# Kernel tuning notes

Measured on AMD Instinct MI355X. Metric: run time of the kernel, lower is better.

Reference implementation:

```python
import jax, jax.numpy as jnp
import numpy as np

D_MODEL = 1024
NUM_HEADS = 16
D_FF = 4096
SEQ = 2048
BATCH = 2
THETA = 10000.0
EPS = 1e-5


def _param(key, shape, fan_in, fan_out):
    std = 2.0 / (fan_in + fan_out) ** 0.5
    return std * jax.random.truncated_normal(key, -3.0, 3.0, shape, dtype=jnp.float32)


def setup_inputs() -> dict:
    key = jax.random.key(0)
    ks = jax.random.split(key, 8)
    d, h, f = D_MODEL, NUM_HEADS, D_FF
    return {
        'x': jax.random.normal(ks[0], (BATCH, SEQ, d), dtype=jnp.float32),
        'token_positions': jnp.arange(SEQ, dtype=jnp.int32),
        'wq': _param(ks[1], (d, d), d, d),
        'wk': _param(ks[2], (d, d), d, d),
        'wv': _param(ks[3], (d, d), d, d),
        'wo': _param(ks[4], (d, d), d, d),
        'ln1_w': jnp.ones((d,), jnp.float32),
        'ln2_w': jnp.ones((d,), jnp.float32),
        'w1': _param(ks[5], (f, d), d, f),
        'w2': _param(ks[6], (d, f), f, d),
        'w3': _param(ks[7], (f, d), d, f),
    }


def rmsnorm(x, w):
    x32 = x.astype(jnp.float32)
    rms = jnp.sqrt(jnp.mean(x32 * x32, axis=-1, keepdims=True) + EPS)
    return ((x32 / rms) * w).astype(x.dtype)


def apply_rope(x, cos, sin):
    # x: [b, h, s, d_k]; cos/sin: [s, d_k//2] -> broadcast as [1,1,s,d_k//2]
    xe, xo = x[..., ::2], x[..., 1::2]
    c = cos[None, None, :, :]
    s = sin[None, None, :, :]
    re = xe * c - xo * s
    ro = xe * s + xo * c
    return jnp.stack((re, ro), axis=-1).reshape(x.shape)


def block_forward(x, token_positions, wq, wk, wv, wo, ln1_w, ln2_w, w1, w2, w3):
    b, s, d = x.shape
    h = NUM_HEADS
    dk = d // h
    # RoPE tables at token positions
    inv_freq = 1.0 / (THETA ** (jnp.arange(0, dk // 2, dtype=jnp.float32) * 2.0 / dk))
    freqs = token_positions.astype(jnp.float32)[:, None] * inv_freq[None, :]  # [s, dk/2]
    cos, sin = jnp.cos(freqs), jnp.sin(freqs)

    # --- attention sublayer (pre-norm) ---
    xn = rmsnorm(x, ln1_w)
    q = jnp.einsum('bsd,ed->bse', xn, wq).reshape(b, s, h, dk).transpose(0, 2, 1, 3)
    k = jnp.einsum('bsd,ed->bse', xn, wk).reshape(b, s, h, dk).transpose(0, 2, 1, 3)
    v = jnp.einsum('bsd,ed->bse', xn, wv).reshape(b, s, h, dk).transpose(0, 2, 1, 3)
    q = apply_rope(q, cos, sin)
    k = apply_rope(k, cos, sin)
    scores = jnp.einsum('bhqd,bhkd->bhqk', q, k) / jnp.sqrt(jnp.float32(dk))
    causal = jnp.tril(jnp.ones((s, s), dtype=bool))
    scores = jnp.where(causal[None, None], scores, -jnp.inf)
    attn = jax.nn.softmax(scores, axis=-1)
    o = jnp.einsum('bhqk,bhkd->bhqd', attn, v)
    o = o.transpose(0, 2, 1, 3).reshape(b, s, d)
    x = x + jnp.einsum('bse,de->bsd', o, wo)

    # --- SwiGLU sublayer (pre-norm) ---
    xn = rmsnorm(x, ln2_w)
    x1 = jnp.einsum('bsd,fd->bsf', xn, w1)
    x3 = jnp.einsum('bsd,fd->bsf', xn, w3)
    gated = (x1 * jax.nn.sigmoid(x1)) * x3
    return x + jnp.einsum('bsf,df->bsd', gated, w2)


def reference(x, token_positions, wq, wk, wv, wo, ln1_w, ln2_w, w1, w2, w3):
    return block_forward(x, token_positions, wq, wk, wv, wo, ln1_w, ln2_w, w1, w2, w3)
```

## Files before the change

### kernel.cpp

```cpp
#include <hip/hip_runtime.h>
#include <hip/hip_bf16.h>

typedef __attribute__((ext_vector_type(4))) float f32x4;
typedef __attribute__((ext_vector_type(8))) short bf16x8;
typedef unsigned short u16;
typedef unsigned int u32;
typedef __attribute__((ext_vector_type(4))) u16 u16x4;

#define DEV static __device__ __forceinline__

constexpr int Bb = 2, Ss = 2048, Dd = 1024, Hh = 16, DKk = 64;
constexpr int Mm = Bb * Ss;

DEV float bf2f(u16 u) { union { u32 i; float f; } v; v.i = (u32)u << 16; return v.f; }
DEV u16 f2bf(float f) {
  union { float f; u32 i; } v; v.f = f;
  u32 r = v.i + 0x7FFFu + ((v.i >> 16) & 1u);
  return (u16)(r >> 16);
}

DEV void gload_lds16(const u16* g, u16* l) {
  __builtin_amdgcn_global_load_lds((const __attribute__((address_space(1))) u32*)g,
                                   (__attribute__((address_space(3))) u32*)l, 16, 0, 0);
}

DEV int swz16(int o) {
  return o ^ (((o >> 8) & 1) << 6) ^ (((o >> 9) & 1) << 5);
}

__global__ __launch_bounds__(256) void k_prep(const float* __restrict__ wq, const float* __restrict__ wk,
                          const float* __restrict__ wv, const float* __restrict__ wo,
                          const float* __restrict__ w1, const float* __restrict__ w2,
                          const float* __restrict__ w3,
                          u16* __restrict__ wqkv, u16* __restrict__ wob,
                          u16* __restrict__ w13, u16* __restrict__ w2b,
                          const float* __restrict__ x, const float* __restrict__ ln1,
                          u16* __restrict__ xn) {
  if (blockIdx.x < 16384) {
    int i = (blockIdx.x * 256 + threadIdx.x) * 4;
    int seg = i >> 20;
    const float* src; u16* dst;
    if (seg == 0)      { src = wq + i;             dst = wqkv + i; }
    else if (seg == 1) { src = wk + (i - (1<<20)); dst = wqkv + i; }
    else if (seg == 2) { src = wv + (i - (2<<20)); dst = wqkv + i; }
    else if (seg == 3) { src = wo + (i - (3<<20)); dst = wob  + (i - (3<<20)); }
    else if (seg < 8)  {
      int ii = i - (4<<20);
      int ri = ii >> 10, ci = ii & 1023;
      int dr = ((ri >> 4) << 5) + (ri & 15);
      src = w1 + ii; dst = w13 + (long)dr * 1024 + ci;
    }
    else if (seg < 12) { src = w2 + (i - (8<<20)); dst = w2b  + (i - (8<<20)); }
    else {
      int ii = i - (12<<20);
      int ri = ii >> 10, ci = ii & 1023;
      int dr = ((ri >> 4) << 5) + 16 + (ri & 15);
      src = w3 + ii; dst = w13 + (long)dr * 1024 + ci;
    }
    float4 v = *(const float4*)src;
    u16x4 o = { f2bf(v.x), f2bf(v.y), f2bf(v.z), f2bf(v.w) };
    *(u16x4*)dst = o;
  } else {
    int row = blockIdx.x - 16384;
    int t = threadIdx.x;
    float4 v = ((const float4*)(x + (long)row * Dd))[t];
    float ss = v.x * v.x + v.y * v.y + v.z * v.z + v.w * v.w;
#pragma unroll
    for (int m = 32; m; m >>= 1) ss += __shfl_xor(ss, m, 64);
    __shared__ float red[4];
    if ((t & 63) == 0) red[t >> 6] = ss;
    __syncthreads();
    float tot = red[0] + red[1] + red[2] + red[3];
    float r = rsqrtf(tot * (1.0f / Dd) + 1e-5f);
    float4 wv2 = ((const float4*)ln1)[t];
    u16x4 o = { f2bf(v.x * r * wv2.x), f2bf(v.y * r * wv2.y),
                f2bf(v.z * r * wv2.z), f2bf(v.w * r * wv2.w) };
    ((u16x4*)(xn + (long)row * Dd))[t] = o;
  }
}

__global__ __launch_bounds__(256) void k_rmsnorm(const float* __restrict__ x,
                                                 const float* __restrict__ w,
                                                 u16* __restrict__ out) {
  int row = blockIdx.x;
  int t = threadIdx.x;
  float4 v = ((const float4*)(x + (long)row * Dd))[t];
  float ss = v.x * v.x + v.y * v.y + v.z * v.z + v.w * v.w;
#pragma unroll
  for (int m = 32; m; m >>= 1) ss += __shfl_xor(ss, m, 64);
  __shared__ float red[4];
  if ((t & 63) == 0) red[t >> 6] = ss;
  __syncthreads();
  float tot = red[0] + red[1] + red[2] + red[3];
  float r = rsqrtf(tot * (1.0f / Dd) + 1e-5f);
  float4 wv = ((const float4*)w)[t];
  u16x4 o = { f2bf(v.x * r * wv.x), f2bf(v.y * r * wv.y),
              f2bf(v.z * r * wv.z), f2bf(v.w * r * wv.w) };
  ((u16x4*)(out + (long)row * Dd))[t] = o;
}

__global__ void k_rope(u16* __restrict__ q, u16* __restrict__ k, const int* __restrict__ tp) {
  int idx = blockIdx.x * 256 + threadIdx.x;
  if (idx >= Bb * Ss * Hh * 32) return;
  int p = idx & 31;
  int h = (idx >> 5) & 15;
  int row = idx >> 9;
  int s = row & (Ss - 1);
  float pos = (float)tp[s];
  float invf = __expf(-(float)p * (2.0f / DKk) * 9.2103403719761836f);
  float fr = pos * invf;
  float sn, cs;
  sincosf(fr, &sn, &cs);
  long base = (long)row * Dd + h * DKk + 2 * p;
  float xe = bf2f(q[base]), xo = bf2f(q[base + 1]);
  q[base]     = f2bf((xe * cs - xo * sn) * 0.125f);
  q[base + 1] = f2bf((xe * sn + xo * cs) * 0.125f);
  xe = bf2f(k[base]); xo = bf2f(k[base + 1]);
  k[base]     = f2bf(xe * cs - xo * sn);
  k[base + 1] = f2bf(xe * sn + xo * cs);
}

__global__ void k_addout4(const u16* __restrict__ p, const float* __restrict__ x2,
                          float* __restrict__ out) {
  int i = (blockIdx.x * 256 + threadIdx.x) * 4;
  float4 c = *(const float4*)(x2 + i);
  float s0 = c.x, s1 = c.y, s2 = c.z, s3 = c.w;
#pragma unroll
  for (int z = 0; z < 4; z++) {
    u16x4 a = *(const u16x4*)(p + (long)z * Mm * 1024 + i);
    s0 += bf2f(a[0]); s1 += bf2f(a[1]); s2 += bf2f(a[2]); s3 += bf2f(a[3]);
  }
  float4 o = { s0, s1, s2, s3 };
  *(float4*)(out + i) = o;
}

template <int OM, bool RES>
__global__ __launch_bounds__(256) void k_gemm(const u16* __restrict__ A,
                                              const u16* __restrict__ Bm,
                                              void* __restrict__ Cout,
                                              const float* __restrict__ Rres,
                                              int N, int Kl, int Kstr) {
  __shared__ u16 Abuf[128 * 32];
  __shared__ u16 Bbuf[128 * 32];
  const int tid = threadIdx.x;
  const int wid = tid >> 6, lane = tid & 63;
  const int wm = wid >> 1, wn = wid & 1;
  const int lq = lane >> 4, ll = lane & 15;
  const int lin = blockIdx.y * gridDim.x + blockIdx.x;
  const int c = lin & 7, j = lin >> 3;
  const int ncc = gridDim.x >> 2;
  const int bxc = (c % ncc) * 4 + (j & 3);
  const int byc = (c / ncc) * 8 + (j >> 2);
  const int m0 = byc * 128, n0 = bxc * 128;

  const u16* Ap = A + (long)blockIdx.z * Kl;
  const u16* Bp = Bm + (long)blockIdx.z * Kl;

  f32x4 acc[4][4] = {};

  const int srow = tid >> 2;
  const int scol = (tid & 3) * 8;
  const long aoff = (long)(m0 + srow) * Kstr + scol;
  const long boff = (long)(n0 + srow) * Kstr + scol;
  u16* aldsw = Abuf + wid * 512;
  u16* bldsw = Bbuf + wid * 512;

  for (int k0 = 0; k0 < Kl; k0 += 32) {
    __syncthreads();
    gload_lds16(Ap + aoff + k0, aldsw);
    gload_lds16(Ap + aoff + (long)64 * Kstr + k0, aldsw + 2048);
    gload_lds16(Bp + boff + k0, bldsw);
    gload_lds16(Bp + boff + (long)64 * Kstr + k0, bldsw + 2048);
    __syncthreads();
    bf16x8 af[4], bfr[4];
#pragma unroll
    for (int i = 0; i < 4; i++)
      af[i] = *(const bf16x8*)&Abuf[(wm * 64 + i * 16 + ll) * 32 + lq * 8];
#pragma unroll
    for (int j2 = 0; j2 < 4; j2++)
      bfr[j2] = *(const bf16x8*)&Bbuf[(wn * 64 + j2 * 16 + ll) * 32 + lq * 8];
#pragma unroll
    for (int i = 0; i < 4; i++)
#pragma unroll
      for (int j2 = 0; j2 < 4; j2++)
        acc[i][j2] = __builtin_amdgcn_mfma_f32_16x16x32_bf16(af[i], bfr[j2], acc[i][j2], 0, 0, 0);
  }

  float* fout = (float*)Cout + (long)blockIdx.z * Mm * (long)N;
#pragma unroll
  for (int i = 0; i < 4; i++) {
    const int rowb = m0 + wm * 64 + i * 16 + lq * 4;
#pragma unroll
    for (int j2 = 0; j2 < 4; j2++) {
      const int col = n0 + wn * 64 + j2 * 16 + ll;
#pragma unroll
      for (int r = 0; r < 4; r++) {
        int rr = rowb + r;
        float v = acc[i][j2][r];
        if (RES) v += Rres[(long)rr * N + col];
        if (OM == 1) {
          fout[(long)rr * N + col] = v;
        } else {
          ((u16*)Cout)[(long)rr * N + col] = f2bf(v);
        }
      }
    }
  }
}

#define STG_A(d, h, kt)                                                         \
  { gload_lds16(A + aoff[0] + (long)(h) * 128 * Kstr + (kt) * 64, &sA[d][h][dst0]); \
    gload_lds16(A + aoff[1] + (long)(h) * 128 * Kstr + (kt) * 64, &sA[d][h][dst1]); }
#define STG_B(d, h, kt)                                                         \
  { gload_lds16(Bm + boff[0] + (long)(h) * 128 * Kstr + (kt) * 64, &sB[d][h][dst0]); \
    gload_lds16(Bm + boff[1] + (long)(h) * 128 * Kstr + (kt) * 64, &sB[d][h][dst1]); }

#define PHASE(q, d, DOB, WVN, ...)                                              \
  {                                                                             \
    bf16x8 af_[2][2];                                                           \
    _Pragma("unroll") for (int s_ = 0; s_ < 2; s_++)                            \
    _Pragma("unroll") for (int kk_ = 0; kk_ < 2; kk_++) {                       \
      int ms_ = (q) * 4 + wm * 2 + s_;                                          \
      int lo_ = ((ms_ & 7) * 16 + ll) * 128 + kk_ * 64 + lq * 16;               \
      af_[s_][kk_] = *(const bf16x8*)((const char*)sA[d][ms_ >> 3] + swz16(lo_)); \
    }                                                                           \
    if (DOB) {                                                                  \
      _Pragma("unroll") for (int ns_ = 0; ns_ < 4; ns_++)                       \
      _Pragma("unroll") for (int kk_ = 0; kk_ < 2; kk_++) {                     \
        int rl_ = wn * 64 + ns_ * 16 + ll;                                      \
        int lo_ = (rl_ & 127) * 128 + kk_ * 64 + lq * 16;                       \
        bfr[ns_][kk_] = *(const bf16x8*)((const char*)sB[d][rl_ >> 7] + swz16(lo_)); \
      }                                                                         \
    }                                                                           \
    __VA_ARGS__;                                                                \
    __builtin_amdgcn_s_barrier();                                               \
    asm volatile("s_waitcnt lgkmcnt(0)" ::: "memory");                          \
    __builtin_amdgcn_sched_barrier(0);                                          \
    __builtin_amdgcn_s_setprio(1);                                              \
    _Pragma("unroll") for (int s_ = 0; s_ < 2; s_++)                            \
    _Pragma("unroll") for (int ns_ = 0; ns_ < 4; ns_++)                         \
    _Pragma("unroll") for (int kk_ = 0; kk_ < 2; kk_++)                         \
      acc[q][s_][ns_] = __builtin_amdgcn_mfma_f32_16x16x32_bf16(                \
          af_[s_][kk_], bfr[ns_][kk_], acc[q][s_][ns_], 0, 0, 0);               \
    __builtin_amdgcn_s_setprio(0);                                              \
    { int wv_ = (WVN);                                                          \
      if (wv_ == 6) { asm volatile("s_waitcnt vmcnt(6)" ::: "memory"); }        \
      else if (wv_ == 0) { asm volatile("s_waitcnt vmcnt(0)" ::: "memory"); } } \
    __builtin_amdgcn_s_barrier();                                               \
  }

template <int OM, int CW, int CH>
__global__ __launch_bounds__(512) void k_gemm8(const u16* __restrict__ A,
                                               const u16* __restrict__ Bm,
                                               void* __restrict__ Cout,
                                               int N, int Kl, int Kstr) {
  __shared__ u16 sA[2][2][8192];
  __shared__ u16 sB[2][2][8192];
  constexpr int NBPC = CW * CH;
  const int gx = gridDim.x;
  const int lin = blockIdx.y * gx + blockIdx.x;
  const int c = lin & 7;
  const int idx = lin >> 3;
  const int chunkid = c + 8 * (idx / NBPC);
  const int jj = idx % NBPC;
  const int ncc = gx / CW;
  const int bx = (chunkid % ncc) * CW + jj % CW;
  const int by = (chunkid / ncc) * CH + jj / CW;
  const long m0 = (long)by * 256, n0 = (long)bx * 256;
  const int tid = threadIdx.x;
  const int wid = tid >> 6, lane = tid & 63;
  const int wm = wid >> 2, wn = wid & 3;
  const int lq = lane >> 4, ll = lane & 15;
  const long zoff = (long)blockIdx.z * Kl;

  long aoff[2], boff[2];
#pragma unroll
  for (int j2 = 0; j2 < 2; j2++) {
    int off = j2 * 8192 + wid * 1024 + lane * 16;
    int lo = swz16(off);
    int r = lo >> 7, cc = (lo & 127) >> 1;
    aoff[j2] = (m0 + r) * Kstr + cc + zoff;
    boff[j2] = (n0 + r) * Kstr + cc + zoff;
  }
  const int dst0 = wid * 512;
  const int dst1 = 4096 + wid * 512;

  f32x4 acc[4][2][4] = {};
  bf16x8 bfr[4][2];

  const int NT = Kl >> 6;
  const int NI = NT >> 1;

  STG_A(0, 0, 0); STG_A(0, 1, 0); STG_B(0, 0, 0); STG_B(0, 1, 0);
  STG_B(1, 0, 1); STG_B(1, 1, 1); STG_A(1, 0, 1);
  asm volatile("s_waitcnt vmcnt(6)" ::: "memory");
  __builtin_amdgcn_s_barrier();

  for (int it = 0; it < NI; it++) {
    const int t = 2 * it;
    const bool full = (t + 2 < NT);
    PHASE(0, 0, true,  -1,            STG_A(1, 1, t + 1))
    PHASE(1, 0, false, -1,            if (full) STG_B(0, 0, t + 2))
    PHASE(2, 0, false, -1,            if (full) STG_B(0, 1, t + 2))
    PHASE(3, 0, false, full ? 6 : 0,  if (full) STG_A(0, 0, t + 2))
    PHASE(0, 1, true,  -1,            if (full) STG_A(0, 1, t + 2))
    PHASE(1, 1, false, -1,            if (full) STG_B(1, 0, t + 3))
    PHASE(2, 1, false, -1,            if (full) STG_B(1, 1, t + 3))
    PHASE(3, 1, false, full ? 6 : -1, if (full) STG_A(1, 0, t + 3))
  }

#pragma unroll
  for (int q = 0; q < 4; q++)
#pragma unroll
    for (int s = 0; s < 2; s++) {
      const long row0 = m0 + (q * 4 + wm * 2 + s) * 16 + lq * 4;
      if (OM == 7) {
#pragma unroll
        for (int n2 = 0; n2 < 2; n2++) {
          const long ocol = ((n0 + wn * 64) >> 1) + n2 * 16 + ll;
#pragma unroll
          for (int r = 0; r < 4; r++) {
            float v1 = acc[q][s][n2 * 2][r];
            float v3 = acc[q][s][n2 * 2 + 1][r];
            float g = v1 / (1.0f + __expf(-v1)) * v3;
            ((u16*)Cout)[(row0 + r) * 4096 + ocol] = f2bf(g);
          }
        }
      } else {
#pragma unroll
        for (int ns = 0; ns < 4; ns++) {
          const long col = n0 + wn * 64 + ns * 16 + ll;
#pragma unroll
          for (int r = 0; r < 4; r++) {
            float v = acc[q][s][ns][r];
            long rr = row0 + r;
            if (OM == 3) {
              if (col < 2048) {
                ((u16*)Cout)[(col >> 10) * (long)(Mm * 1024) + rr * 1024 + (col & 1023)] = f2bf(v);
              } else {
                int d = col & 63, hh = ((int)col >> 6) & 15;
                int b2 = (int)rr >> 11, s2 = (int)rr & (Ss - 1);
                ((u16*)Cout)[(long)(2 * Mm * 1024) + ((long)((b2 * Hh + hh) * DKk + d)) * Ss + s2] = f2bf(v);
              }
            } else {
              ((u16*)Cout)[(long)blockIdx.z * Mm * (long)N + rr * N + col] = f2bf(v);
            }
          }
        }
      }
    }
}

constexpr int PPAD = 80;

DEV void attn_tile(const u16* __restrict__ Kc, const u16* __restrict__ Vc,
                   u16* __restrict__ myP, const bf16x8* qf, f32x4* accO,
                   float* mrow, float* lrow, int qloc, bool diag, int lq, int ll) {
  f32x4 sacc[4] = {};
  __builtin_amdgcn_s_setprio(1);
#pragma unroll
  for (int fn = 0; fn < 4; fn++)
#pragma unroll
    for (int ks = 0; ks < 2; ks++) {
      bf16x8 kf = *(const bf16x8*)&Kc[(fn * 16 + ll) * 64 + (((ks * 4 + lq) ^ (ll & 7)) * 8)];
      sacc[fn] = __builtin_amdgcn_mfma_f32_16x16x32_bf16(qf[ks], kf, sacc[fn], 0, 0, 0);
    }
  __builtin_amdgcn_s_setprio(0);
  float sv[4][4], pmax[4];
#pragma unroll
  for (int r = 0; r < 4; r++) pmax[r] = -1e30f;
#pragma unroll
  for (int fn = 0; fn < 4; fn++) {
    int kc = fn * 16 + ll;
#pragma unroll
    for (int r = 0; r < 4; r++) {
      float v = sacc[fn][r];
      if (diag && kc > qloc + r) v = -1e30f;
      sv[fn][r] = v;
      pmax[r] = fmaxf(pmax[r], v);
    }
  }
#pragma unroll
  for (int r = 0; r < 4; r++) {
#pragma unroll
    for (int m = 1; m < 16; m <<= 1) pmax[r] = fmaxf(pmax[r], __shfl_xor(pmax[r], m, 64));
  }
  float alpha[4], rsum[4];
#pragma unroll
  for (int r = 0; r < 4; r++) {
    float mnew = fmaxf(mrow[r], pmax[r]);
    alpha[r] = __expf(mrow[r] - mnew);
    mrow[r] = mnew;
    rsum[r] = 0.f;
  }
#pragma unroll
  for (int fn = 0; fn < 4; fn++) {
#pragma unroll
    for (int r = 0; r < 4; r++) {
      float p = __expf(sv[fn][r] - mrow[r]);
      rsum[r] += p;
      myP[(lq * 4 + r) * PPAD + fn * 16 + ll] = f2bf(p);
    }
  }
#pragma unroll
  for (int r = 0; r < 4; r++) {
#pragma unroll
    for (int m = 1; m < 16; m <<= 1) rsum[r] += __shfl_xor(rsum[r], m, 64);
    lrow[r] = lrow[r] * alpha[r] + rsum[r];
  }
#pragma unroll
  for (int fn = 0; fn < 4; fn++)
#pragma unroll
    for (int r = 0; r < 4; r++) accO[fn][r] *= alpha[r];
  bf16x8 pa[2];
#pragma unroll
  for (int ks = 0; ks < 2; ks++)
    pa[ks] = *(const bf16x8*)&myP[ll * PPAD + ks * 32 + lq * 8];
  __builtin_amdgcn_s_setprio(1);
#pragma unroll
  for (int fn = 0; fn < 4; fn++)
#pragma unroll
    for (int ks = 0; ks < 2; ks++) {
      bf16x8 vf = *(const bf16x8*)&Vc[(fn * 16 + ll) * 64 + (((ks * 4 + lq) ^ (ll & 7)) * 8)];
      accO[fn] = __builtin_amdgcn_mfma_f32_16x16x32_bf16(pa[ks], vf, accO[fn], 0, 0, 0);
    }
  __builtin_amdgcn_s_setprio(0);
}

__global__ __launch_bounds__(256) void k_attn(const u16* __restrict__ Q,
                                              const u16* __restrict__ Kb,
                                              const u16* __restrict__ VT,
                                              u16* __restrict__ O) {
  __shared__ u16 Kt[2][64 * 64];
  __shared__ u16 Vt[2][64 * 64];
  __shared__ u16 P[4][16 * PPAD];
  const int pair = blockIdx.x;
  const int bh = blockIdx.y;
  const int b = bh >> 4, h = bh & 15;
  const int tid = threadIdx.x;
  const int wid = tid >> 6, lane = tid & 63;
  const int lq = lane >> 4, ll = lane & 15;
  const int qtA = pair, qtB = 31 - pair;
  const int qr0A = qtA * 64 + wid * 16;
  const int qr0B = qtB * 64 + wid * 16;
  const int qloc = wid * 16 + lq * 4;
  const long qkbase = ((long)b * Ss) * Dd + h * DKk;
  const long vbase  = ((long)(b * Hh + h) * DKk) * Ss;
  const int nk = 32 - pair;

  const int slot0 = wid * 64 + lane;
  const int r0 = slot0 >> 3, c0 = (slot0 & 7) ^ (r0 & 7);
  const int slot1 = 256 + slot0;
  const int r1 = slot1 >> 3, c1 = (slot1 & 7) ^ (r1 & 7);
  const int ldsb0 = (wid * 64) * 8;
  const int ldsb1 = (256 + wid * 64) * 8;

  bf16x8 qfA[2], qfB[2];
#pragma unroll
  for (int ks = 0; ks < 2; ks++) {
    qfA[ks] = *(const bf16x8*)&Q[qkbase + (long)(qr0A + ll) * Dd + ks * 32 + lq * 8];
    qfB[ks] = *(const bf16x8*)&Q[qkbase + (long)(qr0B + ll) * Dd + ks * 32 + lq * 8];
  }

  f32x4 accA[4] = {}, accB[4] = {};
  float mA[4], lA[4], mB[4], lB[4];
#pragma unroll
  for (int r = 0; r < 4; r++) { mA[r] = mB[r] = -1e30f; lA[r] = lB[r] = 0.f; }
  u16* myP = P[wid];

  gload_lds16(Kb + qkbase + (long)r0 * Dd + c0 * 8, Kt[0] + ldsb0);
  gload_lds16(Kb + qkbase + (long)r1 * Dd + c1 * 8, Kt[0] + ldsb1);
  gload_lds16(VT + vbase + (long)r0 * Ss + c0 * 8, Vt[0] + ldsb0);
  gload_lds16(VT + vbase + (long)r1 * Ss + c1 * 8, Vt[0] + ldsb1);
  __syncthreads();

  for (int kt = 0; kt < nk; kt++) {
    if (kt + 1 < nk) {
      const int kn = (kt + 1) * 64;
      u16* kd = Kt[(kt + 1) & 1];
      u16* vd = Vt[(kt + 1) & 1];
      gload_lds16(Kb + qkbase + (long)(kn + r0) * Dd + c0 * 8, kd + ldsb0);
      gload_lds16(Kb + qkbase + (long)(kn + r1) * Dd + c1 * 8, kd + ldsb1);
      gload_lds16(VT + vbase + (long)r0 * Ss + kn + c0 * 8, vd + ldsb0);
      gload_lds16(VT + vbase + (long)r1 * Ss + kn + c1 * 8, vd + ldsb1);
    }
    const u16* Kc = Kt[kt & 1];
    const u16* Vc = Vt[kt & 1];

    attn_tile(Kc, Vc, myP, qfB, accB, mB, lB, qloc, kt == nk - 1, lq, ll);
    if (kt <= pair)
      attn_tile(Kc, Vc, myP, qfA, accA, mA, lA, qloc, kt == pair, lq, ll);
    __syncthreads();
  }

#pragma unroll
  for (int fn = 0; fn < 4; fn++) {
#pragma unroll
    for (int r = 0; r < 4; r++) {
      int rowA = qr0A + lq * 4 + r;
      int rowB = qr0B + lq * 4 + r;
      O[((long)(b * Ss + rowA)) * Dd + h * DKk + fn * 16 + ll] = f2bf(accA[fn][r] / lA[r]);
      O[((long)(b * Ss + rowB)) * Dd + h * DKk + fn * 16 + ll] = f2bf(accB[fn][r] / lB[r]);
    }
  }
}

extern "C" void kernel_launch(void* const* d_in, const int* in_sizes, int n_in,
                              void* d_out, int out_size, void* d_ws, size_t ws_size,
                              hipStream_t stream) {
  const float* x   = (const float*)d_in[0];
  const int*   tp  = (const int*)d_in[1];
  const float* wq  = (const float*)d_in[2];
  const float* wk  = (const float*)d_in[3];
  const float* wv  = (const float*)d_in[4];
  const float* wo  = (const float*)d_in[5];
  const float* ln1 = (const float*)d_in[6];
  const float* ln2 = (const float*)d_in[7];
  const float* w1  = (const float*)d_in[8];
  const float* w2  = (const float*)d_in[9];
  const float* w3  = (const float*)d_in[10];

  char* ws = (char*)d_ws;
  const size_t MB = 1024 * 1024;
  u16*   wqkv_b = (u16*)(ws + 0 * MB);
  u16*   wo_b   = (u16*)(ws + 6 * MB);
  u16*   w13_b  = (u16*)(ws + 8 * MB);
  u16*   w2_b   = (u16*)(ws + 24 * MB);
  u16*   xn     = (u16*)(ws + 32 * MB);
  float* x2     = (float*)(ws + 40 * MB);
  u16*   qb     = (u16*)(ws + 56 * MB);
  u16*   kb     = (u16*)(ws + 64 * MB);
  u16*   vtb    = (u16*)(ws + 72 * MB);
  u16*   ob     = (u16*)(ws + 80 * MB);
  u16*   x1     = (u16*)(ws + 56 * MB);
  u16*   pparts = (u16*)(ws + 88 * MB);

  k_prep<<<16384 + Mm, 256, 0, stream>>>(wq, wk, wv, wo, w1, w2, w3,
                                         wqkv_b, wo_b, w13_b, w2_b, x, ln1, xn);
  k_gemm8<3, 3, 4><<<dim3(12, 16), 512, 0, stream>>>(xn, wqkv_b, qb, 3072, 1024, 1024);
  k_rope<<<(Bb * Ss * Hh * 32) / 256, 256, 0, stream>>>(qb, kb, tp);
  k_attn<<<dim3(16, 32), 256, 0, stream>>>(qb, kb, vtb, ob);
  k_gemm<1, true><<<dim3(8, 32), 256, 0, stream>>>(ob, wo_b, x2, x, 1024, 1024, 1024);
  k_rmsnorm<<<Mm, 256, 0, stream>>>(x2, ln2, xn);
  k_gemm8<7, 4, 4><<<dim3(32, 16), 512, 0, stream>>>(xn, w13_b, x1, 8192, 1024, 1024);
  k_gemm8<6, 4, 2><<<dim3(4, 16, 4), 512, 0, stream>>>(x1, w2_b, pparts, 1024, 1024, 4096);
  k_addout4<<<4096, 256, 0, stream>>>(pparts, x2, (float*)d_out);
}
```

Measured before the change: 319.6 us.

## Fuse RoPE into QKV GEMM epilogue and widen attention K/V tiles to 128

Removes the standalone RoPE kernel. k_prep now precomputes cos/sin tables, and the QKV GEMM epilogue applies the rotation (and the 0.125 Q scale) before storing, using a lane shuffle to fetch the paired element. This drops a full read-modify-write pass over Q and K plus a kernel launch. Separately, the attention kernel now stages 128-key K/V tiles per double-buffer stage, so there are half as many barriers and load phases, at the cost of doubled LDS usage. The shuffle-based pairing assumes adjacent columns sit in adjacent lanes in the MFMA output layout. The tables live in the x2 region, which is overwritten later.

```diff
diff --git a/kernel.cpp b/kernel.cpp
--- a/kernel.cpp
+++ b/kernel.cpp
@@ -35,7 +35,8 @@
                           u16* __restrict__ wqkv, u16* __restrict__ wob,
                           u16* __restrict__ w13, u16* __restrict__ w2b,
                           const float* __restrict__ x, const float* __restrict__ ln1,
-                          u16* __restrict__ xn) {
+                          u16* __restrict__ xn, const int* __restrict__ tp,
+                          float* __restrict__ ctab, float* __restrict__ stab) {
   if (blockIdx.x < 16384) {
     int i = (blockIdx.x * 256 + threadIdx.x) * 4;
     int seg = i >> 20;
@@ -60,7 +61,7 @@
     float4 v = *(const float4*)src;
     u16x4 o = { f2bf(v.x), f2bf(v.y), f2bf(v.z), f2bf(v.w) };
     *(u16x4*)dst = o;
-  } else {
+  } else if (blockIdx.x < 16384 + Mm) {
     int row = blockIdx.x - 16384;
     int t = threadIdx.x;
     float4 v = ((const float4*)(x + (long)row * Dd))[t];
@@ -76,6 +77,16 @@
     u16x4 o = { f2bf(v.x * r * wv2.x), f2bf(v.y * r * wv2.y),
                 f2bf(v.z * r * wv2.z), f2bf(v.w * r * wv2.w) };
     ((u16x4*)(xn + (long)row * Dd))[t] = o;
+  } else {
+    int e = (blockIdx.x - 16384 - Mm) * 256 + threadIdx.x;
+    int srow = e >> 5, p = e & 31;
+    float pos = (float)tp[srow];
+    float invf = __expf(-(float)p * (2.0f / DKk) * 9.2103403719761836f);
+    float fr = pos * invf;
+    float sn, cs;
+    sincosf(fr, &sn, &cs);
+    ctab[e] = cs;
+    stab[e] = sn;
   }
 }
 
@@ -97,27 +108,6 @@
   u16x4 o = { f2bf(v.x * r * wv.x), f2bf(v.y * r * wv.y),
               f2bf(v.z * r * wv.z), f2bf(v.w * r * wv.w) };
   ((u16x4*)(out + (long)row * Dd))[t] = o;
-}
-
-__global__ void k_rope(u16* __restrict__ q, u16* __restrict__ k, const int* __restrict__ tp) {
-  int idx = blockIdx.x * 256 + threadIdx.x;
-  if (idx >= Bb * Ss * Hh * 32) return;
-  int p = idx & 31;
-  int h = (idx >> 5) & 15;
-  int row = idx >> 9;
-  int s = row & (Ss - 1);
-  float pos = (float)tp[s];
-  float invf = __expf(-(float)p * (2.0f / DKk) * 9.2103403719761836f);
-  float fr = pos * invf;
-  float sn, cs;
-  sincosf(fr, &sn, &cs);
-  long base = (long)row * Dd + h * DKk + 2 * p;
-  float xe = bf2f(q[base]), xo = bf2f(q[base + 1]);
-  q[base]     = f2bf((xe * cs - xo * sn) * 0.125f);
-  q[base + 1] = f2bf((xe * sn + xo * cs) * 0.125f);
-  xe = bf2f(k[base]); xo = bf2f(k[base + 1]);
-  k[base]     = f2bf(xe * cs - xo * sn);
-  k[base + 1] = f2bf(xe * sn + xo * cs);
 }
 
 __global__ void k_addout4(const u16* __restrict__ p, const float* __restrict__ x2,
@@ -253,6 +243,8 @@
 __global__ __launch_bounds__(512) void k_gemm8(const u16* __restrict__ A,
                                                const u16* __restrict__ Bm,
                                                void* __restrict__ Cout,
+                                               const float* __restrict__ ctab,
+                                               const float* __restrict__ stab,
                                                int N, int Kl, int Kstr) {
   __shared__ u16 sA[2][2][8192];
   __shared__ u16 sB[2][2][8192];
@@ -335,12 +327,22 @@
             float v = acc[q][s][ns][r];
             long rr = row0 + r;
             if (OM == 3) {
+              float v2 = v;
               if (col < 2048) {
-                ((u16*)Cout)[(col >> 10) * (long)(Mm * 1024) + rr * 1024 + (col & 1023)] = f2bf(v);
+                int d = (int)col & 63;
+                int srow = (int)rr & (Ss - 1);
+                int p = d >> 1;
+                float cs = ctab[srow * 32 + p], sn = stab[srow * 32 + p];
+                float o = __shfl_xor(v, 1);
+                v2 = (d & 1) ? (o * sn + v * cs) : (v * cs - o * sn);
+                if (col < 1024) v2 *= 0.125f;
+              }
+              if (col < 2048) {
+                ((u16*)Cout)[(col >> 10) * (long)(Mm * 1024) + rr * 1024 + (col & 1023)] = f2bf(v2);
               } else {
                 int d = col & 63, hh = ((int)col >> 6) & 15;
                 int b2 = (int)rr >> 11, s2 = (int)rr & (Ss - 1);
-                ((u16*)Cout)[(long)(2 * Mm * 1024) + ((long)((b2 * Hh + hh) * DKk + d)) * Ss + s2] = f2bf(v);
+                ((u16*)Cout)[(long)(2 * Mm * 1024) + ((long)((b2 * Hh + hh) * DKk + d)) * Ss + s2] = f2bf(v2);
               }
             } else {
               ((u16*)Cout)[(long)blockIdx.z * Mm * (long)N + rr * N + col] = f2bf(v);
@@ -353,7 +355,7 @@
 
 constexpr int PPAD = 80;
 
-DEV void attn_tile(const u16* __restrict__ Kc, const u16* __restrict__ Vc,
+DEV void attn_tile(const u16* __restrict__ Kh, const u16* __restrict__ Vc, int vcb,
                    u16* __restrict__ myP, const bf16x8* qf, f32x4* accO,
                    float* mrow, float* lrow, int qloc, bool diag, int lq, int ll) {
   f32x4 sacc[4] = {};
@@ -362,7 +364,7 @@
   for (int fn = 0; fn < 4; fn++)
 #pragma unroll
     for (int ks = 0; ks < 2; ks++) {
-      bf16x8 kf = *(const bf16x8*)&Kc[(fn * 16 + ll) * 64 + (((ks * 4 + lq) ^ (ll & 7)) * 8)];
+      bf16x8 kf = *(const bf16x8*)&Kh[(fn * 16 + ll) * 64 + (((ks * 4 + lq) ^ (ll & 7)) * 8)];
       sacc[fn] = __builtin_amdgcn_mfma_f32_16x16x32_bf16(qf[ks], kf, sacc[fn], 0, 0, 0);
     }
   __builtin_amdgcn_s_setprio(0);
@@ -421,7 +423,7 @@
   for (int fn = 0; fn < 4; fn++)
 #pragma unroll
     for (int ks = 0; ks < 2; ks++) {
-      bf16x8 vf = *(const bf16x8*)&Vc[(fn * 16 + ll) * 64 + (((ks * 4 + lq) ^ (ll & 7)) * 8)];
+      bf16x8 vf = *(const bf16x8*)&Vc[(fn * 16 + ll) * 128 + (((vcb + ks * 4 + lq) ^ (ll & 7)) * 8)];
       accO[fn] = __builtin_amdgcn_mfma_f32_16x16x32_bf16(pa[ks], vf, accO[fn], 0, 0, 0);
     }
   __builtin_amdgcn_s_setprio(0);
@@ -431,8 +433,8 @@
                                               const u16* __restrict__ Kb,
                                               const u16* __restrict__ VT,
                                               u16* __restrict__ O) {
-  __shared__ u16 Kt[2][64 * 64];
-  __shared__ u16 Vt[2][64 * 64];
+  __shared__ u16 Kt[2][128 * 64];
+  __shared__ u16 Vt[2][64 * 128];
   __shared__ u16 P[4][16 * PPAD];
   const int pair = blockIdx.x;
   const int bh = blockIdx.y;
@@ -446,14 +448,17 @@
   const int qloc = wid * 16 + lq * 4;
   const long qkbase = ((long)b * Ss) * Dd + h * DKk;
   const long vbase  = ((long)(b * Hh + h) * DKk) * Ss;
-  const int nk = 32 - pair;
-
-  const int slot0 = wid * 64 + lane;
-  const int r0 = slot0 >> 3, c0 = (slot0 & 7) ^ (r0 & 7);
-  const int slot1 = 256 + slot0;
-  const int r1 = slot1 >> 3, c1 = (slot1 & 7) ^ (r1 & 7);
-  const int ldsb0 = (wid * 64) * 8;
-  const int ldsb1 = (256 + wid * 64) * 8;
+  const int nk64 = 32 - pair;
+  const int nk128 = (nk64 + 1) >> 1;
+
+  int kr[4], kc[4], vr[4], vc[4], ldsb[4];
+#pragma unroll
+  for (int i = 0; i < 4; i++) {
+    int s = 256 * i + wid * 64 + lane;
+    kr[i] = s >> 3;  kc[i] = (s & 7) ^ (kr[i] & 7);
+    vr[i] = s >> 4;  vc[i] = (s & 15) ^ (vr[i] & 7);
+    ldsb[i] = (256 * i + wid * 64) * 8;
+  }
 
   bf16x8 qfA[2], qfB[2];
 #pragma unroll
@@ -468,28 +473,36 @@
   for (int r = 0; r < 4; r++) { mA[r] = mB[r] = -1e30f; lA[r] = lB[r] = 0.f; }
   u16* myP = P[wid];
 
-  gload_lds16(Kb + qkbase + (long)r0 * Dd + c0 * 8, Kt[0] + ldsb0);
-  gload_lds16(Kb + qkbase + (long)r1 * Dd + c1 * 8, Kt[0] + ldsb1);
-  gload_lds16(VT + vbase + (long)r0 * Ss + c0 * 8, Vt[0] + ldsb0);
-  gload_lds16(VT + vbase + (long)r1 * Ss + c1 * 8, Vt[0] + ldsb1);
+#pragma unroll
+  for (int i = 0; i < 4; i++) {
+    gload_lds16(Kb + qkbase + (long)kr[i] * Dd + kc[i] * 8, Kt[0] + ldsb[i]);
+    gload_lds16(VT + vbase + (long)vr[i] * Ss + vc[i] * 8, Vt[0] + ldsb[i]);
+  }
   __syncthreads();
 
-  for (int kt = 0; kt < nk; kt++) {
-    if (kt + 1 < nk) {
-      const int kn = (kt + 1) * 64;
-      u16* kd = Kt[(kt + 1) & 1];
-      u16* vd = Vt[(kt + 1) & 1];
-      gload_lds16(Kb + qkbase + (long)(kn + r0) * Dd + c0 * 8, kd + ldsb0);
-      gload_lds16(Kb + qkbase + (long)(kn + r1) * Dd + c1 * 8, kd + ldsb1);
-      gload_lds16(VT + vbase + (long)r0 * Ss + kn + c0 * 8, vd + ldsb0);
-      gload_lds16(VT + vbase + (long)r1 * Ss + kn + c1 * 8, vd + ldsb1);
-    }
-    const u16* Kc = Kt[kt & 1];
-    const u16* Vc = Vt[kt & 1];
-
-    attn_tile(Kc, Vc, myP, qfB, accB, mB, lB, qloc, kt == nk - 1, lq, ll);
-    if (kt <= pair)
-      attn_tile(Kc, Vc, myP, qfA, accA, mA, lA, qloc, kt == pair, lq, ll);
+  for (int j = 0; j < nk128; j++) {
+    if (j + 1 < nk128) {
+      const int kn = (j + 1) * 128;
+      u16* kd = Kt[(j + 1) & 1];
+      u16* vd = Vt[(j + 1) & 1];
+#pragma unroll
+      for (int i = 0; i < 4; i++) {
+        gload_lds16(Kb + qkbase + (long)(kn + kr[i]) * Dd + kc[i] * 8, kd + ldsb[i]);
+        gload_lds16(VT + vbase + (long)vr[i] * Ss + kn + vc[i] * 8, vd + ldsb[i]);
+      }
+    }
+    const u16* Kc = Kt[j & 1];
+    const u16* Vc = Vt[j & 1];
+#pragma unroll
+    for (int hh = 0; hh < 2; hh++) {
+      const int kt64 = 2 * j + hh;
+      if (kt64 < nk64)
+        attn_tile(Kc + hh * 64 * 64, Vc, hh * 8, myP, qfB, accB, mB, lB, qloc,
+                  kt64 == nk64 - 1, lq, ll);
+      if (kt64 <= pair)
+        attn_tile(Kc + hh * 64 * 64, Vc, hh * 8, myP, qfA, accA, mA, lA, qloc,
+                  kt64 == pair, lq, ll);
+    }
     __syncthreads();
   }
 
@@ -528,6 +541,8 @@
   u16*   w2_b   = (u16*)(ws + 24 * MB);
   u16*   xn     = (u16*)(ws + 32 * MB);
   float* x2     = (float*)(ws + 40 * MB);
+  float* ctab   = (float*)(ws + 40 * MB);
+  float* stab   = ctab + 65536;
   u16*   qb     = (u16*)(ws + 56 * MB);
   u16*   kb     = (u16*)(ws + 64 * MB);
   u16*   vtb    = (u16*)(ws + 72 * MB);
@@ -535,14 +550,14 @@
   u16*   x1     = (u16*)(ws + 56 * MB);
   u16*   pparts = (u16*)(ws + 88 * MB);
 
-  k_prep<<<16384 + Mm, 256, 0, stream>>>(wq, wk, wv, wo, w1, w2, w3,
-                                         wqkv_b, wo_b, w13_b, w2_b, x, ln1, xn);
-  k_gemm8<3, 3, 4><<<dim3(12, 16), 512, 0, stream>>>(xn, wqkv_b, qb, 3072, 1024, 1024);
-  k_rope<<<(Bb * Ss * Hh * 32) / 256, 256, 0, stream>>>(qb, kb, tp);
+  k_prep<<<16384 + Mm + 256, 256, 0, stream>>>(wq, wk, wv, wo, w1, w2, w3,
+                                               wqkv_b, wo_b, w13_b, w2_b,
+                                               x, ln1, xn, tp, ctab, stab);
+  k_gemm8<3, 3, 4><<<dim3(12, 16), 512, 0, stream>>>(xn, wqkv_b, qb, ctab, stab, 3072, 1024, 1024);
   k_attn<<<dim3(16, 32), 256, 0, stream>>>(qb, kb, vtb, ob);
   k_gemm<1, true><<<dim3(8, 32), 256, 0, stream>>>(ob, wo_b, x2, x, 1024, 1024, 1024);
   k_rmsnorm<<<Mm, 256, 0, stream>>>(x2, ln2, xn);
-  k_gemm8<7, 4, 4><<<dim3(32, 16), 512, 0, stream>>>(xn, w13_b, x1, 8192, 1024, 1024);
-  k_gemm8<6, 4, 2><<<dim3(4, 16, 4), 512, 0, stream>>>(x1, w2_b, pparts, 1024, 1024, 4096);
+  k_gemm8<7, 4, 4><<<dim3(32, 16), 512, 0, stream>>>(xn, w13_b, x1, nullptr, nullptr, 8192, 1024, 1024);
+  k_gemm8<6, 4, 2><<<dim3(4, 16, 4), 512, 0, stream>>>(x1, w2_b, pparts, nullptr, nullptr, 1024, 1024, 4096);
   k_addout4<<<4096, 256, 0, stream>>>(pparts, x2, (float*)d_out);
 }
```

New measurement: 365.3 us. +14.3%, slower.
